# Kernel optimization log

Hardware: AMD Instinct MI355X
Metric: run time of the kernel (lower is better)

Reference implementation:

```python
import jax, jax.numpy as jnp
import numpy as np

N_NODES = 50000
N_EDGES = 800000
D = 128
LN_EPS = 1e-5


def setup_inputs() -> dict:
    key = jax.random.key(0)
    ks = jax.random.split(key, 8)
    s = 1.0 / np.sqrt(D)
    return {
        "x": jax.random.normal(ks[0], (N_NODES, D), jnp.float32),
        "edge_index": jax.random.randint(ks[1], (2, N_EDGES), 0, N_NODES, jnp.int64),
        "W1l": jax.random.normal(ks[2], (D, D), jnp.float32) * s,
        "b1l": jnp.zeros((D,), jnp.float32),
        "W1r": jax.random.normal(ks[3], (D, D), jnp.float32) * s,
        "W2l": jax.random.normal(ks[4], (D, D), jnp.float32) * s,
        "b2l": jnp.zeros((D,), jnp.float32),
        "W2r": jax.random.normal(ks[5], (D, D), jnp.float32) * s,
        "ln_w": jnp.ones((D,), jnp.float32),
        "ln_b": jnp.zeros((D,), jnp.float32),
    }


def _sage_conv(h, edge_index, Wl, bl, Wr):
    # PyG SAGEConv (mean aggr): out = lin_l(mean_{j in N(i)} h_j) + lin_r(h_i)
    src, dst = edge_index[0], edge_index[1]
    n = h.shape[0]
    msg_sum = jax.ops.segment_sum(h[src], dst, num_segments=n)      # [N, D]
    cnt = jax.ops.segment_sum(jnp.ones_like(src, h.dtype), dst, num_segments=n)
    mean = msg_sum / jnp.maximum(cnt, 1.0)[:, None]                  # 0 for isolated
    return mean @ Wl.T + bl + h @ Wr.T


def _layer_norm(h, w, b):
    mu = jnp.mean(h, axis=-1, keepdims=True)
    var = jnp.mean(jnp.square(h - mu), axis=-1, keepdims=True)
    return (h - mu) * jax.lax.rsqrt(var + LN_EPS) * w + b


def reference(x, edge_index, W1l, b1l, W1r, W2l, b2l, W2r, ln_w, ln_b):
    h = jax.nn.relu(_sage_conv(x, edge_index, W1l, b1l, W1r))
    h = jax.nn.relu(_sage_conv(h, edge_index, W2l, b2l, W2r))
    return _layer_norm(h, ln_w, ln_b)
```

## Files before the change

### kernel.cpp

```cpp
#include <hip/hip_runtime.h>

#define DN 128
#define LS 136

typedef short s16x8 __attribute__((ext_vector_type(8)));
typedef float f32x4 __attribute__((ext_vector_type(4)));

__device__ __forceinline__ float bf2f(unsigned short u) {
    union { unsigned int i; float f; } v; v.i = ((unsigned int)u) << 16; return v.f;
}
__device__ __forceinline__ unsigned short f2bf(float f) {
    union { float f; unsigned int i; } v; v.f = f;
    unsigned int r = v.i + 0x7fffu + ((v.i >> 16) & 1u);
    return (unsigned short)(r >> 16);
}
__device__ __forceinline__ float lo16(unsigned int u) { return bf2f((unsigned short)(u & 0xffffu)); }
__device__ __forceinline__ float hi16(unsigned int u) { return bf2f((unsigned short)(u >> 16)); }
__device__ __forceinline__ unsigned int pack2(float x, float y) {
    return (unsigned int)f2bf(x) | ((unsigned int)f2bf(y) << 16);
}
__device__ __forceinline__ float ldx(const void* p, size_t i, int f32) {
    return f32 ? ((const float*)p)[i] : bf2f(((const unsigned short*)p)[i]);
}

__global__ void k_diag(unsigned short* out, int cnt, float val) {
    unsigned short v = f2bf(val);
    for (int i = blockIdx.x * blockDim.x + threadIdx.x; i < cnt; i += gridDim.x * blockDim.x)
        out[i] = v;
}

__global__ void k_probe(const void* x, const void* w, const int* e, int* flags) {
    int g = blockIdx.x * 256 + threadIdx.x;
    const unsigned short* xu = (const unsigned short*)x;
    int hitx = 0, hitw = 0, hite = 0;
    for (int i = g; i < 65536; i += 32768)
        if ((xu[i] & 0x7F80u) == 0x7F80u) hitx = 1;
    const unsigned short* wu = (const unsigned short*)w;
    if (g < 16384 && (wu[g] & 0x7F80u) == 0x7F80u) hitw = 1;
    if (g < 1000 && e[2 * g + 1] != 0) hite = 1;
    if (hitx) atomicOr(&flags[0], 1);
    if (hitw) atomicOr(&flags[2], 1);
    if (hite) atomicOr(&flags[1], 1);
}

__global__ void k_cast(const void* x, const int* xflagp, unsigned int* xb, int cnt) {
    int i = blockIdx.x * blockDim.x + threadIdx.x;
    if (i >= cnt) return;
    if (*xflagp) {
        float2 v = *(const float2*)((const float*)x + 2 * (size_t)i);
        xb[i] = pack2(v.x, v.y);
    } else {
        xb[i] = ((const unsigned int*)x)[i];
    }
}


__global__ __launch_bounds__(1024) void k_packhist(const int* e, const int* flags,
        unsigned int* packed, int* cnt, int E, int n) {
    __shared__ int hist[256];
    int t = threadIdx.x;
    int b0 = blockIdx.x * 4096;
    if (t < 256) hist[t] = 0;
    __syncthreads();
    int is64 = (flags[1] == 0);
#pragma unroll
    for (int k = 0; k < 4; ++k) {
        int i = b0 + t + k * 1024;
        if (i < E) {
            int d = is64 ? e[2 * (E + i)] : e[E + i];
            int s = is64 ? e[2 * i] : e[i];
            if ((unsigned)s >= (unsigned)n) s = 0;
            unsigned int key = ((unsigned)d < (unsigned)n)
                             ? (((unsigned)d << 16) | (unsigned)s)
                             : 0xFFFF0000u;
            packed[i] = key;
            atomicAdd(&hist[key >> 24], 1);
        }
    }
    __syncthreads();
    if (t < 256 && hist[t]) atomicAdd(&cnt[t], hist[t]);
}

__global__ void k_s256(const int* cnt, int* base, int* cursor, int* rowp, int n) {
    __shared__ int buf[256];
    int t = threadIdx.x;
    int v = cnt[t];
    buf[t] = v;
    __syncthreads();
    for (int off = 1; off < 256; off <<= 1) {
        int add = (t >= off) ? buf[t - off] : 0;
        __syncthreads();
        buf[t] += add;
        __syncthreads();
    }
    base[t] = buf[t] - v;
    cursor[t] = buf[t] - v;
    if (t == 255) base[256] = buf[255];
    if (t == 195) rowp[n] = buf[195];
}

__global__ __launch_bounds__(1024) void k_p1scat(const unsigned int* in, int* gcur,
                                                 unsigned int* out, int E) {
    __shared__ int hist[256], lcur[256], gbase[256];
    int t = threadIdx.x;
    int b0 = blockIdx.x * 4096;
    int nb = E - b0; if (nb > 4096) nb = 4096;
    if (t < 256) hist[t] = 0;
    __syncthreads();
    unsigned int v[4];
#pragma unroll
    for (int k = 0; k < 4; ++k) {
        int i = t + k * 1024;
        v[k] = (i < nb) ? in[b0 + i] : 0u;
        if (i < nb) atomicAdd(&hist[v[k] >> 24], 1);
    }
    __syncthreads();
    if (t < 256) {
        lcur[t] = 0;
        if (hist[t]) gbase[t] = atomicAdd(&gcur[t], hist[t]);
    }
    __syncthreads();
#pragma unroll
    for (int k = 0; k < 4; ++k) {
        int i = t + k * 1024;
        if (i < nb) {
            unsigned int d = v[k] >> 24;
            int p = atomicAdd(&lcur[d], 1);
            out[gbase[d] + p] = v[k];
        }
    }
}

__global__ __launch_bounds__(1024) void k_p2(const unsigned int* in, const int* base,
                                             int* rowp, int* col, int n) {
    __shared__ int hist[256], cur[256];
    int t = threadIdx.x;
    int b = blockIdx.x;
    int lo = base[b], hi = base[b + 1];
    if (t < 256) hist[t] = 0;
    __syncthreads();
    for (int i = lo + t; i < hi; i += 1024)
        atomicAdd(&hist[(in[i] >> 16) & 0xFFu], 1);
    __syncthreads();
    if (t < 64) {
        int h0 = hist[4 * t], h1 = hist[4 * t + 1], h2 = hist[4 * t + 2], h3 = hist[4 * t + 3];
        int tot = h0 + h1 + h2 + h3;
        int pre = tot;
#pragma unroll
        for (int off = 1; off < 64; off <<= 1) {
            int u = __shfl_up(pre, off, 64);
            if (t >= off) pre += u;
        }
        int e0 = pre - tot;
        int e1 = e0 + h0, e2 = e1 + h1, e3 = e2 + h2;
        cur[4 * t] = e0; cur[4 * t + 1] = e1; cur[4 * t + 2] = e2; cur[4 * t + 3] = e3;
        int d0 = b * 256 + 4 * t;
        if (d0 < n)     rowp[d0]     = lo + e0;
        if (d0 + 1 < n) rowp[d0 + 1] = lo + e1;
        if (d0 + 2 < n) rowp[d0 + 2] = lo + e2;
        if (d0 + 3 < n) rowp[d0 + 3] = lo + e3;
    }
    __syncthreads();
    for (int i = lo + t; i < hi; i += 1024) {
        unsigned int v = in[i];
        int p = atomicAdd(&cur[(v >> 16) & 0xFFu], 1);
        col[lo + p] = (int)(v & 0xFFFFu);
    }
}

__global__ void k_gather(const int* rowp, const int* col, const unsigned int* hp,
                         unsigned int* M, int n) {
    int row = blockIdx.x * 4 + (threadIdx.x >> 6);
    if (row >= n) return;
    const int L = threadIdx.x & 63;
    int b = rowp[row], e = rowp[row + 1];
    float s0 = 0.f, s1 = 0.f;
    for (int base = b; base < e; base += 64) {
        int cnt = e - base; if (cnt > 64) cnt = 64;
        int myc = (L < cnt) ? col[base + L] : 0;
        int j = 0;
        for (; j + 8 <= cnt; j += 8) {
            int a0 = __shfl(myc, j + 0, 64);
            int a1 = __shfl(myc, j + 1, 64);
            int a2 = __shfl(myc, j + 2, 64);
            int a3 = __shfl(myc, j + 3, 64);
            int a4 = __shfl(myc, j + 4, 64);
            int a5 = __shfl(myc, j + 5, 64);
            int a6 = __shfl(myc, j + 6, 64);
            int a7 = __shfl(myc, j + 7, 64);
            unsigned int u0 = hp[(size_t)a0 * 64 + L];
            unsigned int u1 = hp[(size_t)a1 * 64 + L];
            unsigned int u2 = hp[(size_t)a2 * 64 + L];
            unsigned int u3 = hp[(size_t)a3 * 64 + L];
            unsigned int u4 = hp[(size_t)a4 * 64 + L];
            unsigned int u5 = hp[(size_t)a5 * 64 + L];
            unsigned int u6 = hp[(size_t)a6 * 64 + L];
            unsigned int u7 = hp[(size_t)a7 * 64 + L];
            s0 += lo16(u0); s1 += hi16(u0);
            s0 += lo16(u1); s1 += hi16(u1);
            s0 += lo16(u2); s1 += hi16(u2);
            s0 += lo16(u3); s1 += hi16(u3);
            s0 += lo16(u4); s1 += hi16(u4);
            s0 += lo16(u5); s1 += hi16(u5);
            s0 += lo16(u6); s1 += hi16(u6);
            s0 += lo16(u7); s1 += hi16(u7);
        }
        for (; j + 4 <= cnt; j += 4) {
            int a0 = __shfl(myc, j + 0, 64);
            int a1 = __shfl(myc, j + 1, 64);
            int a2 = __shfl(myc, j + 2, 64);
            int a3 = __shfl(myc, j + 3, 64);
            unsigned int u0 = hp[(size_t)a0 * 64 + L];
            unsigned int u1 = hp[(size_t)a1 * 64 + L];
            unsigned int u2 = hp[(size_t)a2 * 64 + L];
            unsigned int u3 = hp[(size_t)a3 * 64 + L];
            s0 += lo16(u0); s1 += hi16(u0);
            s0 += lo16(u1); s1 += hi16(u1);
            s0 += lo16(u2); s1 += hi16(u2);
            s0 += lo16(u3); s1 += hi16(u3);
        }
        for (; j < cnt; ++j) {
            int s = __shfl(myc, j, 64);
            unsigned int u = hp[(size_t)s * 64 + L];
            s0 += lo16(u); s1 += hi16(u);
        }
    }
    int d = e - b; if (d < 1) d = 1;
    float inv = 1.0f / (float)d;
    M[(size_t)row * 64 + L] = pack2(s0 * inv, s1 * inv);
}

__global__ __launch_bounds__(256) void k_gemm(
        const unsigned int* M, const unsigned int* hin,
        const void* Wl, const void* Wr, const void* bias, const int* flags,
        void* hout, int n, int do_ln, const void* lnw, const void* lnb) {
    __shared__ unsigned short sA[64 * LS];
    __shared__ unsigned short sB[128 * LS];
    unsigned int* sAu = (unsigned int*)sA;
    unsigned int* sBu = (unsigned int*)sB;
    const int t = threadIdx.x;
    const int wf32 = flags[2];
    const int i0 = blockIdx.x * 64;
    const int lane = t & 63, wv = t >> 6, ln15 = lane & 15, quad = lane >> 4;

    f32x4 acc[8];
#pragma unroll
    for (int i = 0; i < 8; ++i) { f32x4 z = {0.f, 0.f, 0.f, 0.f}; acc[i] = z; }

    for (int phase = 0; phase < 2; ++phase) {
        const unsigned int* A = phase ? hin : M;
#pragma unroll
        for (int i = 0; i < 16; ++i) {
            int idx = t + i * 256, r = idx >> 6, c = idx & 63;
            int node = i0 + r;
            sAu[r * 68 + c] = (node < n) ? A[(size_t)node * 64 + c] : 0u;
        }
        const void* W = phase ? Wr : Wl;
        if (wf32) {
            const float* wp = (const float*)W;
#pragma unroll
            for (int i = 0; i < 32; ++i) {
                int idx = t + i * 256, r = idx >> 6, kk = idx & 63;
                float2 f = *(const float2*)(wp + (size_t)r * DN + 2 * kk);
                sBu[r * 68 + kk] = pack2(f.x, f.y);
            }
        } else {
            const unsigned int* wp = (const unsigned int*)W;
#pragma unroll
            for (int i = 0; i < 32; ++i) {
                int idx = t + i * 256, r = idx >> 6, kk = idx & 63;
                sBu[r * 68 + kk] = wp[(size_t)r * 64 + kk];
            }
        }
        __syncthreads();

        const int mrow = wv * 16;
#pragma unroll
        for (int ks = 0; ks < 4; ++ks) {
            s16x8 a = *(const s16x8*)&sA[(mrow + ln15) * LS + ks * 32 + quad * 8];
#pragma unroll
            for (int nt = 0; nt < 8; ++nt) {
                s16x8 b = *(const s16x8*)&sB[(nt * 16 + ln15) * LS + ks * 32 + quad * 8];
                acc[nt] = __builtin_amdgcn_mfma_f32_16x16x32_bf16(a, b, acc[nt], 0, 0, 0);
            }
        }
        __syncthreads();
    }

#pragma unroll
    for (int nt = 0; nt < 8; ++nt) {
        float bs = ldx(bias, nt * 16 + ln15, wf32);
#pragma unroll
        for (int r = 0; r < 4; ++r) {
            float v = acc[nt][r] + bs;
            acc[nt][r] = (v > 0.f) ? v : 0.f;
        }
    }

    if (!do_ln) {
#pragma unroll
        for (int nt = 0; nt < 8; ++nt) {
            int colv = nt * 16 + ln15;
#pragma unroll
            for (int r = 0; r < 4; ++r) {
                int node = i0 + wv * 16 + quad * 4 + r;
                if (node < n)
                    ((unsigned short*)hout)[(size_t)node * DN + colv] = f2bf(acc[nt][r]);
            }
        }
        return;
    }

    const int mix = (flags[0] != flags[2]);
    if (mix) {
#pragma unroll
        for (int nt = 0; nt < 8; ++nt) {
            int colv = nt * 16 + ln15;
#pragma unroll
            for (int r = 0; r < 4; ++r) {
                int node = i0 + wv * 16 + quad * 4 + r;
                if (node < n)
                    ((unsigned short*)hout)[(size_t)node * DN + colv] = 0x442F;
            }
        }
        return;
    }
    const int outf32 = (flags[0] && flags[2]);
    float lw[8], lb[8];
#pragma unroll
    for (int nt = 0; nt < 8; ++nt) {
        lw[nt] = ldx(lnw, nt * 16 + ln15, wf32);
        lb[nt] = ldx(lnb, nt * 16 + ln15, wf32);
    }
#pragma unroll
    for (int r = 0; r < 4; ++r) {
        float s = 0.f;
#pragma unroll
        for (int nt = 0; nt < 8; ++nt) s += acc[nt][r];
#pragma unroll
        for (int off = 1; off < 16; off <<= 1) s += __shfl_xor(s, off, 64);
        float mu = s * (1.0f / 128.0f);
        float q = 0.f;
#pragma unroll
        for (int nt = 0; nt < 8; ++nt) { float d = acc[nt][r] - mu; q += d * d; }
#pragma unroll
        for (int off = 1; off < 16; off <<= 1) q += __shfl_xor(q, off, 64);
        float rs = rsqrtf(q * (1.0f / 128.0f) + 1e-5f);
        int node = i0 + wv * 16 + quad * 4 + r;
        if (node < n) {
#pragma unroll
            for (int nt = 0; nt < 8; ++nt) {
                int colv = nt * 16 + ln15;
                float o = (acc[nt][r] - mu) * rs * lw[nt] + lb[nt];
                if (outf32) ((float*)hout)[(size_t)node * DN + colv] = o;
                else ((unsigned short*)hout)[(size_t)node * DN + colv] = f2bf(o);
            }
        }
    }
}

extern "C" void kernel_launch(void* const* d_in, const int* in_sizes, int n_in,
                              void* d_out, int out_size, void* d_ws, size_t ws_size,
                              hipStream_t stream) {
    const int N_EXP = 50000, E_EXP = 800000;

    const size_t sz_flags  = 256;
    const size_t sz_rowp   = (((size_t)(N_EXP + 1) * 4) + 255) & ~(size_t)255;
    const size_t sz_cursor = (((size_t)N_EXP * 4) + 255) & ~(size_t)255;
    const size_t sz_col    = (((size_t)E_EXP * 4) + 255) & ~(size_t)255;
    const size_t sz_M      = (size_t)N_EXP * 64 * 4;
    const size_t sz_h      = (size_t)N_EXP * DN * 2;
    const size_t need = sz_flags + sz_rowp + sz_cursor + sz_col + sz_M + sz_h;

    float diag = 0.f;
    if (in_sizes[0] != N_EXP * DN) diag += 1000.f;
    if (in_sizes[1] != 2 * E_EXP)  diag += 2000.f;
    if (n_in != 10)                diag += 4000.f;
    if (out_size != N_EXP * DN)    diag += 8000.f;
    if (ws_size < need)            diag += 16000.f;
    if (diag != 0.f) {
        k_diag<<<1024, 256, 0, stream>>>((unsigned short*)d_out, N_EXP * DN, diag);
        return;
    }

    const void* x   = d_in[0];
    const int*  ei  = (const int*)d_in[1];
    const void* W1l = d_in[2];
    const void* b1l = d_in[3];
    const void* W1r = d_in[4];
    const void* W2l = d_in[5];
    const void* b2l = d_in[6];
    const void* W2r = d_in[7];
    const void* lnw = d_in[8];
    const void* lnb = d_in[9];

    const int n = N_EXP, E = E_EXP;

    char* ws = (char*)d_ws;
    int* flags  = (int*)ws;
    int* rowp   = (int*)(ws + sz_flags);
    int* small  = (int*)(ws + sz_flags + sz_rowp);
    int* col    = (int*)(ws + sz_flags + sz_rowp + sz_cursor);
    unsigned int* M  = (unsigned int*)(ws + sz_flags + sz_rowp + sz_cursor + sz_col);
    unsigned int* h1 = (unsigned int*)(ws + sz_flags + sz_rowp + sz_cursor + sz_col + sz_M);

    int* cnt   = (int*)(ws + sz_flags);
    int* bbase = small;
    int* bcur  = small + 260;
    unsigned int* packed0 = (unsigned int*)col;
    unsigned int* packed1 = (unsigned int*)M;

    hipMemsetAsync(ws, 0, 1280, stream);

    k_probe<<<128, 256, 0, stream>>>(x, W1l, ei, flags);

    int P1B = (E + 4095) / 4096;
    k_packhist<<<P1B, 1024, 0, stream>>>(ei, flags, packed0, cnt, E, n);
    k_s256<<<1, 256, 0, stream>>>(cnt, bbase, bcur, rowp, n);
    k_p1scat<<<P1B, 1024, 0, stream>>>(packed0, bcur, packed1, E);
    k_p2<<<P1B, 1024, 0, stream>>>(packed1, bbase, rowp, col, n);

    int cc = n * 64;
    k_cast<<<(cc + 255) / 256, 256, 0, stream>>>(x, &flags[0], h1, cc);

    int gb = (n + 3) / 4;
    int mb = (n + 63) / 64;

    k_gather<<<gb, 256, 0, stream>>>(rowp, col, h1, M, n);
    k_gemm<<<mb, 256, 0, stream>>>(M, h1, W1l, W1r, b1l, flags, h1, n, 0, nullptr, nullptr);
    k_gather<<<gb, 256, 0, stream>>>(rowp, col, h1, M, n);
    k_gemm<<<mb, 256, 0, stream>>>(M, h1, W2l, W2r, b2l, flags, d_out, n, 1, lnw, lnb);
}
```

Before: 255.9 us.

## Fuse CSR build into one cooperative kernel and widen gather loads

Replaces the memset, probe, histogram, scan, scatter, bucket-sort and cast launches with a single cooperative kernel that uses grid-wide syncs between phases. Edge keys stay in registers instead of round-tripping through a packed buffer. The original multi-kernel path is kept as a fallback if the cooperative launch fails. The gather kernel now has each half-wavefront fetch a different neighbor with 8-byte loads and combines the halves with a cross-lane shuffle. The aim is lower launch overhead, fewer global writes and more bytes in flight per load, at the cost of grid-sync latency and a fixed 196-block grid.

```diff
diff --git a/kernel.cpp b/kernel.cpp
--- a/kernel.cpp
+++ b/kernel.cpp
@@ -1,4 +1,7 @@
 #include <hip/hip_runtime.h>
+#include <hip/hip_cooperative_groups.h>
+
+namespace cg = cooperative_groups;
 
 #define DN 128
 #define LS 136
@@ -27,6 +30,138 @@
     unsigned short v = f2bf(val);
     for (int i = blockIdx.x * blockDim.x + threadIdx.x; i < cnt; i += gridDim.x * blockDim.x)
         out[i] = v;
+}
+
+__global__ __launch_bounds__(1024) void k_build(
+        const void* x, const int* e, const void* w1,
+        int* flags, int* cnt, int* bbase, int* bcur,
+        unsigned int* scat, int* rowp, int* col, unsigned int* h1,
+        int E, int n, int cc) {
+    cg::grid_group grid = cg::this_grid();
+    __shared__ int hist[256], aux[256], gb[256];
+    const int t = threadIdx.x, b = blockIdx.x;
+
+    if (b == 0) {
+        if (t < 64) flags[t] = 0;
+        if (t < 256) cnt[t] = 0;
+    }
+    grid.sync();
+
+    if (b < 32) {
+        int g = b * 1024 + t;
+        const unsigned short* xu = (const unsigned short*)x;
+        int hitx = 0;
+        for (int i = g; i < 65536; i += 32768)
+            if ((xu[i] & 0x7F80u) == 0x7F80u) hitx = 1;
+        if (hitx) atomicOr(&flags[0], 1);
+        const unsigned short* wu = (const unsigned short*)w1;
+        if (g < 16384 && (wu[g] & 0x7F80u) == 0x7F80u) atomicOr(&flags[2], 1);
+        if (g < 1000 && e[2 * g + 1] != 0) atomicOr(&flags[1], 1);
+    }
+    grid.sync();
+
+    const int is64 = (flags[1] == 0);
+    const int xf = flags[0];
+
+    if (t < 256) hist[t] = 0;
+    __syncthreads();
+    unsigned int v[4];
+    const int e0 = b * 4096;
+#pragma unroll
+    for (int k = 0; k < 4; ++k) {
+        int i = e0 + t + k * 1024;
+        if (i < E) {
+            int d = is64 ? e[2 * (E + i)] : e[E + i];
+            int s = is64 ? e[2 * i] : e[i];
+            if ((unsigned)s >= (unsigned)n) s = 0;
+            unsigned int key = ((unsigned)d < (unsigned)n)
+                             ? (((unsigned)d << 16) | (unsigned)s) : 0xFFFF0000u;
+            v[k] = key;
+            atomicAdd(&hist[key >> 24], 1);
+        }
+    }
+    __syncthreads();
+    if (t < 256 && hist[t]) atomicAdd(&cnt[t], hist[t]);
+    if (xf) {
+        const float* xp = (const float*)x;
+        for (int i = b * 1024 + t; i < cc; i += 196 * 1024) {
+            float2 f = *(const float2*)(xp + 2 * (size_t)i);
+            h1[i] = pack2(f.x, f.y);
+        }
+    } else {
+        const unsigned int* xp = (const unsigned int*)x;
+        for (int i = b * 1024 + t; i < cc; i += 196 * 1024)
+            h1[i] = xp[i];
+    }
+    grid.sync();
+
+    if (b == 0) {
+        int vv = (t < 256) ? cnt[t] : 0;
+        if (t < 256) aux[t] = vv;
+        __syncthreads();
+        for (int off = 1; off < 256; off <<= 1) {
+            int add = (t < 256 && t >= off) ? aux[t - off] : 0;
+            __syncthreads();
+            if (t < 256) aux[t] += add;
+            __syncthreads();
+        }
+        if (t < 256) {
+            int ex = aux[t] - vv;
+            bbase[t] = ex;
+            bcur[t] = ex;
+            if (t == 196) rowp[n] = ex;
+        }
+    }
+    grid.sync();
+
+    if (t < 256) {
+        aux[t] = 0;
+        gb[t] = hist[t] ? atomicAdd(&bcur[t], hist[t]) : 0;
+    }
+    __syncthreads();
+#pragma unroll
+    for (int k = 0; k < 4; ++k) {
+        int i = e0 + t + k * 1024;
+        if (i < E) {
+            unsigned int d = v[k] >> 24;
+            int p = atomicAdd(&aux[d], 1);
+            scat[gb[d] + p] = v[k];
+        }
+    }
+    grid.sync();
+
+    {
+        int lo = bbase[b], hi = bbase[b + 1];
+        if (t < 256) hist[t] = 0;
+        __syncthreads();
+        for (int i = lo + t; i < hi; i += 1024)
+            atomicAdd(&hist[(scat[i] >> 16) & 0xFFu], 1);
+        __syncthreads();
+        if (t < 64) {
+            int h0 = hist[4 * t], h1_ = hist[4 * t + 1];
+            int h2 = hist[4 * t + 2], h3 = hist[4 * t + 3];
+            int tot = h0 + h1_ + h2 + h3;
+            int pre = tot;
+#pragma unroll
+            for (int off = 1; off < 64; off <<= 1) {
+                int u = __shfl_up(pre, off, 64);
+                if (t >= off) pre += u;
+            }
+            int q0 = pre - tot, q1 = q0 + h0, q2 = q1 + h1_, q3 = q2 + h2;
+            aux[4 * t] = q0; aux[4 * t + 1] = q1; aux[4 * t + 2] = q2; aux[4 * t + 3] = q3;
+            int d0 = b * 256 + 4 * t;
+            if (d0 < n)     rowp[d0]     = lo + q0;
+            if (d0 + 1 < n) rowp[d0 + 1] = lo + q1;
+            if (d0 + 2 < n) rowp[d0 + 2] = lo + q2;
+            if (d0 + 3 < n) rowp[d0 + 3] = lo + q3;
+        }
+        __syncthreads();
+        for (int i = lo + t; i < hi; i += 1024) {
+            unsigned int w = scat[i];
+            int p = atomicAdd(&aux[(w >> 16) & 0xFFu], 1);
+            col[lo + p] = (int)(w & 0xFFFFu);
+        }
+    }
 }
 
 __global__ void k_probe(const void* x, const void* w, const int* e, int* flags) {
@@ -42,7 +177,6 @@
     if (hitw) atomicOr(&flags[2], 1);
     if (hite) atomicOr(&flags[1], 1);
 }
-
 __global__ void k_cast(const void* x, const int* xflagp, unsigned int* xb, int cnt) {
     int i = blockIdx.x * blockDim.x + threadIdx.x;
     if (i >= cnt) return;
@@ -53,8 +187,6 @@
         xb[i] = ((const unsigned int*)x)[i];
     }
 }
-
-
 __global__ __launch_bounds__(1024) void k_packhist(const int* e, const int* flags,
         unsigned int* packed, int* cnt, int E, int n) {
     __shared__ int hist[256];
@@ -71,8 +203,7 @@
             int s = is64 ? e[2 * i] : e[i];
             if ((unsigned)s >= (unsigned)n) s = 0;
             unsigned int key = ((unsigned)d < (unsigned)n)
-                             ? (((unsigned)d << 16) | (unsigned)s)
-                             : 0xFFFF0000u;
+                             ? (((unsigned)d << 16) | (unsigned)s) : 0xFFFF0000u;
             packed[i] = key;
             atomicAdd(&hist[key >> 24], 1);
         }
@@ -80,7 +211,6 @@
     __syncthreads();
     if (t < 256 && hist[t]) atomicAdd(&cnt[t], hist[t]);
 }
-
 __global__ void k_s256(const int* cnt, int* base, int* cursor, int* rowp, int n) {
     __shared__ int buf[256];
     int t = threadIdx.x;
@@ -98,7 +228,6 @@
     if (t == 255) base[256] = buf[255];
     if (t == 195) rowp[n] = buf[195];
 }
-
 __global__ __launch_bounds__(1024) void k_p1scat(const unsigned int* in, int* gcur,
                                                  unsigned int* out, int E) {
     __shared__ int hist[256], lcur[256], gbase[256];
@@ -130,7 +259,6 @@
         }
     }
 }
-
 __global__ __launch_bounds__(1024) void k_p2(const unsigned int* in, const int* base,
                                              int* rowp, int* col, int n) {
     __shared__ int hist[256], cur[256];
@@ -168,66 +296,55 @@
     }
 }
 
+#define G_IDX(o) int a##o = __shfl(myc, j + 2 * o + h, 64);
+#define G_LD(o)  uint2 u##o = hp2[(size_t)a##o * 32 + l5];
+#define G_AC(o)  s00 += lo16(u##o.x); s01 += hi16(u##o.x); \
+                 s10 += lo16(u##o.y); s11 += hi16(u##o.y);
 __global__ void k_gather(const int* rowp, const int* col, const unsigned int* hp,
                          unsigned int* M, int n) {
     int row = blockIdx.x * 4 + (threadIdx.x >> 6);
     if (row >= n) return;
     const int L = threadIdx.x & 63;
+    const int h = L >> 5, l5 = L & 31;
+    const uint2* hp2 = (const uint2*)hp;
     int b = rowp[row], e = rowp[row + 1];
-    float s0 = 0.f, s1 = 0.f;
+    float s00 = 0.f, s01 = 0.f, s10 = 0.f, s11 = 0.f;
     for (int base = b; base < e; base += 64) {
         int cnt = e - base; if (cnt > 64) cnt = 64;
         int myc = (L < cnt) ? col[base + L] : 0;
         int j = 0;
-        for (; j + 8 <= cnt; j += 8) {
-            int a0 = __shfl(myc, j + 0, 64);
-            int a1 = __shfl(myc, j + 1, 64);
-            int a2 = __shfl(myc, j + 2, 64);
-            int a3 = __shfl(myc, j + 3, 64);
-            int a4 = __shfl(myc, j + 4, 64);
-            int a5 = __shfl(myc, j + 5, 64);
-            int a6 = __shfl(myc, j + 6, 64);
-            int a7 = __shfl(myc, j + 7, 64);
-            unsigned int u0 = hp[(size_t)a0 * 64 + L];
-            unsigned int u1 = hp[(size_t)a1 * 64 + L];
-            unsigned int u2 = hp[(size_t)a2 * 64 + L];
-            unsigned int u3 = hp[(size_t)a3 * 64 + L];
-            unsigned int u4 = hp[(size_t)a4 * 64 + L];
-            unsigned int u5 = hp[(size_t)a5 * 64 + L];
-            unsigned int u6 = hp[(size_t)a6 * 64 + L];
-            unsigned int u7 = hp[(size_t)a7 * 64 + L];
-            s0 += lo16(u0); s1 += hi16(u0);
-            s0 += lo16(u1); s1 += hi16(u1);
-            s0 += lo16(u2); s1 += hi16(u2);
-            s0 += lo16(u3); s1 += hi16(u3);
-            s0 += lo16(u4); s1 += hi16(u4);
-            s0 += lo16(u5); s1 += hi16(u5);
-            s0 += lo16(u6); s1 += hi16(u6);
-            s0 += lo16(u7); s1 += hi16(u7);
+        for (; j + 16 <= cnt; j += 16) {
+            G_IDX(0) G_IDX(1) G_IDX(2) G_IDX(3) G_IDX(4) G_IDX(5) G_IDX(6) G_IDX(7)
+            G_LD(0) G_LD(1) G_LD(2) G_LD(3) G_LD(4) G_LD(5) G_LD(6) G_LD(7)
+            G_AC(0) G_AC(1) G_AC(2) G_AC(3) G_AC(4) G_AC(5) G_AC(6) G_AC(7)
         }
         for (; j + 4 <= cnt; j += 4) {
-            int a0 = __shfl(myc, j + 0, 64);
-            int a1 = __shfl(myc, j + 1, 64);
-            int a2 = __shfl(myc, j + 2, 64);
-            int a3 = __shfl(myc, j + 3, 64);
-            unsigned int u0 = hp[(size_t)a0 * 64 + L];
-            unsigned int u1 = hp[(size_t)a1 * 64 + L];
-            unsigned int u2 = hp[(size_t)a2 * 64 + L];
-            unsigned int u3 = hp[(size_t)a3 * 64 + L];
-            s0 += lo16(u0); s1 += hi16(u0);
-            s0 += lo16(u1); s1 += hi16(u1);
-            s0 += lo16(u2); s1 += hi16(u2);
-            s0 += lo16(u3); s1 += hi16(u3);
-        }
-        for (; j < cnt; ++j) {
-            int s = __shfl(myc, j, 64);
-            unsigned int u = hp[(size_t)s * 64 + L];
-            s0 += lo16(u); s1 += hi16(u);
-        }
-    }
+            G_IDX(0) G_IDX(1)
+            G_LD(0) G_LD(1)
+            G_AC(0) G_AC(1)
+        }
+        for (; j < cnt; j += 2) {
+            int idx = j + h;
+            int valid = idx < cnt;
+            int a = __shfl(myc, valid ? idx : j, 64);
+            uint2 u = hp2[(size_t)a * 32 + l5];
+            float m = valid ? 1.f : 0.f;
+            s00 += m * lo16(u.x); s01 += m * hi16(u.x);
+            s10 += m * lo16(u.y); s11 += m * hi16(u.y);
+        }
+    }
+    s00 += __shfl_xor(s00, 32, 64);
+    s01 += __shfl_xor(s01, 32, 64);
+    s10 += __shfl_xor(s10, 32, 64);
+    s11 += __shfl_xor(s11, 32, 64);
     int d = e - b; if (d < 1) d = 1;
     float inv = 1.0f / (float)d;
-    M[(size_t)row * 64 + L] = pack2(s0 * inv, s1 * inv);
+    if (h == 0) {
+        uint2 o;
+        o.x = pack2(s00 * inv, s01 * inv);
+        o.y = pack2(s10 * inv, s11 * inv);
+        ((uint2*)M)[(size_t)row * 32 + l5] = o;
+    }
 }
 
 __global__ __launch_bounds__(256) void k_gemm(
@@ -395,6 +512,7 @@
     const void* lnb = d_in[9];
 
     const int n = N_EXP, E = E_EXP;
+    int cc = n * 64;
 
     char* ws = (char*)d_ws;
     int* flags  = (int*)ws;
@@ -404,24 +522,30 @@
     unsigned int* M  = (unsigned int*)(ws + sz_flags + sz_rowp + sz_cursor + sz_col);
     unsigned int* h1 = (unsigned int*)(ws + sz_flags + sz_rowp + sz_cursor + sz_col + sz_M);
 
-    int* cnt   = (int*)(ws + sz_flags);
-    int* bbase = small;
-    int* bcur  = small + 260;
-    unsigned int* packed0 = (unsigned int*)col;
-    unsigned int* packed1 = (unsigned int*)M;
-
-    hipMemsetAsync(ws, 0, 1280, stream);
-
-    k_probe<<<128, 256, 0, stream>>>(x, W1l, ei, flags);
-
-    int P1B = (E + 4095) / 4096;
-    k_packhist<<<P1B, 1024, 0, stream>>>(ei, flags, packed0, cnt, E, n);
-    k_s256<<<1, 256, 0, stream>>>(cnt, bbase, bcur, rowp, n);
-    k_p1scat<<<P1B, 1024, 0, stream>>>(packed0, bcur, packed1, E);
-    k_p2<<<P1B, 1024, 0, stream>>>(packed1, bbase, rowp, col, n);
-
-    int cc = n * 64;
-    k_cast<<<(cc + 255) / 256, 256, 0, stream>>>(x, &flags[0], h1, cc);
+    int* cnt   = small;
+    int* bbase = small + 256;
+    int* bcur  = small + 520;
+    unsigned int* scat = (unsigned int*)M;
+
+    {
+        void* xa = (void*)x; void* ea = (void*)ei; void* wa = (void*)W1l;
+        void* args[] = { &xa, &ea, &wa, &flags, &cnt, &bbase, &bcur,
+                         &scat, &rowp, &col, &h1, (void*)&E, (void*)&n, (void*)&cc };
+        hipError_t err = hipLaunchCooperativeKernel(
+            reinterpret_cast<void*>(k_build), dim3(196), dim3(1024), args, 0, stream);
+        if (err != hipSuccess) {
+            unsigned int* packed0 = (unsigned int*)col;
+            hipMemsetAsync(flags, 0, sz_flags, stream);
+            hipMemsetAsync(cnt, 0, 1024, stream);
+            k_probe<<<128, 256, 0, stream>>>(x, W1l, ei, flags);
+            int P1B = (E + 4095) / 4096;
+            k_packhist<<<P1B, 1024, 0, stream>>>(ei, flags, packed0, cnt, E, n);
+            k_s256<<<1, 256, 0, stream>>>(cnt, bbase, bcur, rowp, n);
+            k_p1scat<<<P1B, 1024, 0, stream>>>(packed0, bcur, scat, E);
+            k_p2<<<P1B, 1024, 0, stream>>>(scat, bbase, rowp, col, n);
+            k_cast<<<(cc + 255) / 256, 256, 0, stream>>>(x, &flags[0], h1, cc);
+        }
+    }
 
     int gb = (n + 3) / 4;
     int mb = (n + 63) / 64;
```

Measured after the change: 375.6 us. 46.8% more time.

## Fold input/weight casts into packhist, drop scan kernel, vectorize GEMM tile loads

Applied to the files above, without the earlier changes.

Merges the x-to-bf16 cast and a one-time weight/bias/LN-parameter conversion into the edge packing/histogram kernel. The 256-bucket prefix scan now runs inside the scatter kernels instead of in its own launch, which removes two launches. The GEMM now loads A and B tiles with 128-bit loads from the pre-converted bf16 weights, so each block no longer re-converts fp32 weights. The risk is that the fused packhist kernel does more serial work per thread, and every block repeats the redundant scan.

```diff
diff --git a/kernel.cpp b/kernel.cpp
--- a/kernel.cpp
+++ b/kernel.cpp
@@ -43,26 +43,24 @@
     if (hite) atomicOr(&flags[1], 1);
 }
 
-__global__ void k_cast(const void* x, const int* xflagp, unsigned int* xb, int cnt) {
-    int i = blockIdx.x * blockDim.x + threadIdx.x;
-    if (i >= cnt) return;
-    if (*xflagp) {
-        float2 v = *(const float2*)((const float*)x + 2 * (size_t)i);
-        xb[i] = pack2(v.x, v.y);
-    } else {
-        xb[i] = ((const unsigned int*)x)[i];
-    }
-}
-
-
-__global__ __launch_bounds__(1024) void k_packhist(const int* e, const int* flags,
-        unsigned int* packed, int* cnt, int E, int n) {
+
+__global__ __launch_bounds__(1024) void k_packhist(
+        const int* e, const void* x,
+        const void* W1l, const void* W1r, const void* W2l, const void* W2r,
+        const void* b1l, const void* b2l, const void* lnw, const void* lnb,
+        const int* flags, unsigned int* packed, int* cnt,
+        unsigned int* h1, unsigned int* wb, float* biasf, float* lnf,
+        int E, int n, int cc) {
     __shared__ int hist[256];
-    int t = threadIdx.x;
-    int b0 = blockIdx.x * 4096;
+    const int t = threadIdx.x, b = blockIdx.x;
+    const int nthr = gridDim.x * 1024;
+    const int g = b * 1024 + t;
     if (t < 256) hist[t] = 0;
     __syncthreads();
-    int is64 = (flags[1] == 0);
+    const int is64 = (flags[1] == 0);
+    const int xf = flags[0];
+    const int wf = flags[2];
+    const int b0 = b * 4096;
 #pragma unroll
     for (int k = 0; k < 4; ++k) {
         int i = b0 + t + k * 1024;
@@ -71,37 +69,64 @@
             int s = is64 ? e[2 * i] : e[i];
             if ((unsigned)s >= (unsigned)n) s = 0;
             unsigned int key = ((unsigned)d < (unsigned)n)
-                             ? (((unsigned)d << 16) | (unsigned)s)
-                             : 0xFFFF0000u;
+                             ? (((unsigned)d << 16) | (unsigned)s) : 0xFFFF0000u;
             packed[i] = key;
             atomicAdd(&hist[key >> 24], 1);
         }
     }
+    if (xf) {
+        const float* xp = (const float*)x;
+        for (int i = g; i < cc; i += nthr) {
+            float2 f = *(const float2*)(xp + 2 * (size_t)i);
+            h1[i] = pack2(f.x, f.y);
+        }
+    } else {
+        const unsigned int* xp = (const unsigned int*)x;
+        for (int i = g; i < cc; i += nthr) h1[i] = xp[i];
+    }
+    for (int i = g; i < 32768; i += nthr) {
+        int m = i >> 13, el = i & 8191;
+        const void* W = (m == 0) ? W1l : (m == 1) ? W1r : (m == 2) ? W2l : W2r;
+        unsigned int v;
+        if (wf) {
+            float2 f = *(const float2*)((const float*)W + 2 * (size_t)el);
+            v = pack2(f.x, f.y);
+        } else {
+            v = ((const unsigned int*)W)[el];
+        }
+        wb[(size_t)m * 8192 + el] = v;
+    }
+    if (g < 512) {
+        float v;
+        if (g < 128)      v = ldx(b1l, g, wf);
+        else if (g < 256) v = ldx(b2l, g - 128, wf);
+        else if (g < 384) v = ldx(lnw, g - 256, wf);
+        else              v = ldx(lnb, g - 384, wf);
+        if (g < 256) biasf[g] = v; else lnf[g - 256] = v;
+    }
     __syncthreads();
     if (t < 256 && hist[t]) atomicAdd(&cnt[t], hist[t]);
 }
 
-__global__ void k_s256(const int* cnt, int* base, int* cursor, int* rowp, int n) {
-    __shared__ int buf[256];
-    int t = threadIdx.x;
-    int v = cnt[t];
-    buf[t] = v;
-    __syncthreads();
-    for (int off = 1; off < 256; off <<= 1) {
-        int add = (t >= off) ? buf[t - off] : 0;
-        __syncthreads();
-        buf[t] += add;
-        __syncthreads();
-    }
-    base[t] = buf[t] - v;
-    cursor[t] = buf[t] - v;
-    if (t == 255) base[256] = buf[255];
-    if (t == 195) rowp[n] = buf[195];
-}
-
-__global__ __launch_bounds__(1024) void k_p1scat(const unsigned int* in, int* gcur,
-                                                 unsigned int* out, int E) {
-    __shared__ int hist[256], lcur[256], gbase[256];
+__device__ __forceinline__ void scan_cnt(const int* cnt, int* sbase, int t) {
+    if (t < 64) {
+        int c0 = cnt[4 * t], c1 = cnt[4 * t + 1], c2 = cnt[4 * t + 2], c3 = cnt[4 * t + 3];
+        int tot = c0 + c1 + c2 + c3, pre = tot;
+#pragma unroll
+        for (int off = 1; off < 64; off <<= 1) {
+            int u = __shfl_up(pre, off, 64);
+            if (t >= off) pre += u;
+        }
+        int e0 = pre - tot;
+        sbase[4 * t] = e0; sbase[4 * t + 1] = e0 + c0;
+        sbase[4 * t + 2] = e0 + c0 + c1; sbase[4 * t + 3] = e0 + c0 + c1 + c2;
+        if (t == 63) sbase[256] = pre;
+    }
+}
+
+__global__ __launch_bounds__(1024) void k_p1scat(const unsigned int* in, const int* cnt,
+                                                 int* rsv, unsigned int* out, int E) {
+    __shared__ int hist[256], lcur[256], gbase[256], sbase[257];
     int t = threadIdx.x;
     int b0 = blockIdx.x * 4096;
     int nb = E - b0; if (nb > 4096) nb = 4096;
@@ -114,10 +139,11 @@
         v[k] = (i < nb) ? in[b0 + i] : 0u;
         if (i < nb) atomicAdd(&hist[v[k] >> 24], 1);
     }
+    scan_cnt(cnt, sbase, t);
     __syncthreads();
     if (t < 256) {
         lcur[t] = 0;
-        if (hist[t]) gbase[t] = atomicAdd(&gcur[t], hist[t]);
+        if (hist[t]) gbase[t] = sbase[t] + atomicAdd(&rsv[t], hist[t]);
     }
     __syncthreads();
 #pragma unroll
@@ -131,14 +157,16 @@
     }
 }
 
-__global__ __launch_bounds__(1024) void k_p2(const unsigned int* in, const int* base,
+__global__ __launch_bounds__(1024) void k_p2(const unsigned int* in, const int* cnt,
                                              int* rowp, int* col, int n) {
-    __shared__ int hist[256], cur[256];
+    __shared__ int hist[256], cur[256], sbase[257];
     int t = threadIdx.x;
     int b = blockIdx.x;
-    int lo = base[b], hi = base[b + 1];
     if (t < 256) hist[t] = 0;
-    __syncthreads();
+    scan_cnt(cnt, sbase, t);
+    __syncthreads();
+    int lo = sbase[b], hi = sbase[b + 1];
+    if (b == 0 && t == 0) rowp[n] = sbase[196];
     for (int i = lo + t; i < hi; i += 1024)
         atomicAdd(&hist[(in[i] >> 16) & 0xFFu], 1);
     __syncthreads();
@@ -232,14 +260,14 @@
 
 __global__ __launch_bounds__(256) void k_gemm(
         const unsigned int* M, const unsigned int* hin,
-        const void* Wl, const void* Wr, const void* bias, const int* flags,
-        void* hout, int n, int do_ln, const void* lnw, const void* lnb) {
+        const unsigned int* wbl, const unsigned int* wbr,
+        const float* biasf, const int* flags,
+        void* hout, int n, int do_ln, const float* lnwf, const float* lnbf) {
     __shared__ unsigned short sA[64 * LS];
     __shared__ unsigned short sB[128 * LS];
     unsigned int* sAu = (unsigned int*)sA;
     unsigned int* sBu = (unsigned int*)sB;
     const int t = threadIdx.x;
-    const int wf32 = flags[2];
     const int i0 = blockIdx.x * 64;
     const int lane = t & 63, wv = t >> 6, ln15 = lane & 15, quad = lane >> 4;
 
@@ -250,27 +278,18 @@
     for (int phase = 0; phase < 2; ++phase) {
         const unsigned int* A = phase ? hin : M;
 #pragma unroll
-        for (int i = 0; i < 16; ++i) {
-            int idx = t + i * 256, r = idx >> 6, c = idx & 63;
+        for (int i = 0; i < 4; ++i) {
+            int idx = t + i * 256, r = idx >> 4, c4 = (idx & 15) * 4;
             int node = i0 + r;
-            sAu[r * 68 + c] = (node < n) ? A[(size_t)node * 64 + c] : 0u;
-        }
-        const void* W = phase ? Wr : Wl;
-        if (wf32) {
-            const float* wp = (const float*)W;
-#pragma unroll
-            for (int i = 0; i < 32; ++i) {
-                int idx = t + i * 256, r = idx >> 6, kk = idx & 63;
-                float2 f = *(const float2*)(wp + (size_t)r * DN + 2 * kk);
-                sBu[r * 68 + kk] = pack2(f.x, f.y);
-            }
-        } else {
-            const unsigned int* wp = (const unsigned int*)W;
-#pragma unroll
-            for (int i = 0; i < 32; ++i) {
-                int idx = t + i * 256, r = idx >> 6, kk = idx & 63;
-                sBu[r * 68 + kk] = wp[(size_t)r * 64 + kk];
-            }
+            uint4 v = make_uint4(0u, 0u, 0u, 0u);
+            if (node < n) v = *(const uint4*)(A + (size_t)node * 64 + c4);
+            *(uint4*)(sAu + r * 68 + c4) = v;
+        }
+        const unsigned int* W = phase ? wbr : wbl;
+#pragma unroll
+        for (int i = 0; i < 8; ++i) {
+            int idx = t + i * 256, r = idx >> 4, c4 = (idx & 15) * 4;
+            *(uint4*)(sBu + r * 68 + c4) = *(const uint4*)(W + (size_t)r * 64 + c4);
         }
         __syncthreads();
 
@@ -280,8 +299,8 @@
             s16x8 a = *(const s16x8*)&sA[(mrow + ln15) * LS + ks * 32 + quad * 8];
 #pragma unroll
             for (int nt = 0; nt < 8; ++nt) {
-                s16x8 b = *(const s16x8*)&sB[(nt * 16 + ln15) * LS + ks * 32 + quad * 8];
-                acc[nt] = __builtin_amdgcn_mfma_f32_16x16x32_bf16(a, b, acc[nt], 0, 0, 0);
+                s16x8 bfr = *(const s16x8*)&sB[(nt * 16 + ln15) * LS + ks * 32 + quad * 8];
+                acc[nt] = __builtin_amdgcn_mfma_f32_16x16x32_bf16(a, bfr, acc[nt], 0, 0, 0);
             }
         }
         __syncthreads();
@@ -289,7 +308,7 @@
 
 #pragma unroll
     for (int nt = 0; nt < 8; ++nt) {
-        float bs = ldx(bias, nt * 16 + ln15, wf32);
+        float bs = biasf[nt * 16 + ln15];
 #pragma unroll
         for (int r = 0; r < 4; ++r) {
             float v = acc[nt][r] + bs;
@@ -329,8 +348,8 @@
     float lw[8], lb[8];
 #pragma unroll
     for (int nt = 0; nt < 8; ++nt) {
-        lw[nt] = ldx(lnw, nt * 16 + ln15, wf32);
-        lb[nt] = ldx(lnb, nt * 16 + ln15, wf32);
+        lw[nt] = lnwf[nt * 16 + ln15];
+        lb[nt] = lnbf[nt * 16 + ln15];
     }
 #pragma unroll
     for (int r = 0; r < 4; ++r) {
@@ -395,39 +414,42 @@
     const void* lnb = d_in[9];
 
     const int n = N_EXP, E = E_EXP;
+    int cc = n * 64;
 
     char* ws = (char*)d_ws;
-    int* flags  = (int*)ws;
     int* rowp   = (int*)(ws + sz_flags);
     int* small  = (int*)(ws + sz_flags + sz_rowp);
     int* col    = (int*)(ws + sz_flags + sz_rowp + sz_cursor);
     unsigned int* M  = (unsigned int*)(ws + sz_flags + sz_rowp + sz_cursor + sz_col);
     unsigned int* h1 = (unsigned int*)(ws + sz_flags + sz_rowp + sz_cursor + sz_col + sz_M);
 
-    int* cnt   = (int*)(ws + sz_flags);
-    int* bbase = small;
-    int* bcur  = small + 260;
+    int* flags = small;
+    int* cnt   = small + 64;
+    int* rsv   = small + 320;
+    unsigned int* wb    = (unsigned int*)(small + 576);
+    float* biasf = (float*)(small + 33344);
+    float* lnf   = (float*)(small + 33600);
     unsigned int* packed0 = (unsigned int*)col;
     unsigned int* packed1 = (unsigned int*)M;
 
-    hipMemsetAsync(ws, 0, 1280, stream);
+    hipMemsetAsync(small, 0, 2304, stream);
 
     k_probe<<<128, 256, 0, stream>>>(x, W1l, ei, flags);
 
     int P1B = (E + 4095) / 4096;
-    k_packhist<<<P1B, 1024, 0, stream>>>(ei, flags, packed0, cnt, E, n);
-    k_s256<<<1, 256, 0, stream>>>(cnt, bbase, bcur, rowp, n);
-    k_p1scat<<<P1B, 1024, 0, stream>>>(packed0, bcur, packed1, E);
-    k_p2<<<P1B, 1024, 0, stream>>>(packed1, bbase, rowp, col, n);
-
-    int cc = n * 64;
-    k_cast<<<(cc + 255) / 256, 256, 0, stream>>>(x, &flags[0], h1, cc);
+    k_packhist<<<P1B, 1024, 0, stream>>>(ei, x, W1l, W1r, W2l, W2r,
+                                         b1l, b2l, lnw, lnb, flags,
+                                         packed0, cnt, h1, wb, biasf, lnf, E, n, cc);
+    k_p1scat<<<P1B, 1024, 0, stream>>>(packed0, cnt, rsv, packed1, E);
+    k_p2<<<P1B, 1024, 0, stream>>>(packed1, cnt, rowp, col, n);
 
     int gb = (n + 3) / 4;
     int mb = (n + 63) / 64;
 
     k_gather<<<gb, 256, 0, stream>>>(rowp, col, h1, M, n);
-    k_gemm<<<mb, 256, 0, stream>>>(M, h1, W1l, W1r, b1l, flags, h1, n, 0, nullptr, nullptr);
+    k_gemm<<<mb, 256, 0, stream>>>(M, h1, wb, wb + 8192, biasf, flags,
+                                   h1, n, 0, nullptr, nullptr);
     k_gather<<<gb, 256, 0, stream>>>(rowp, col, h1, M, n);
-    k_gemm<<<mb, 256, 0, stream>>>(M, h1, W2l, W2r, b2l, flags, d_out, n, 1, lnw, lnb);
-}
+    k_gemm<<<mb, 256, 0, stream>>>(M, h1, wb + 16384, wb + 24576, biasf + 128, flags,
+                                   d_out, n, 1, lnf, lnf + 128);
+}
```

Result: faster. 211.2 us (-17.5%).
